# Kernel optimization log

Hardware: AMD Instinct MI355X
Metric: run time of the kernel (lower is better)

Reference implementation:

```python
import jax, jax.numpy as jnp
import numpy as np

N_NODES = 100000
N_EDGES = 1600000
IN_DIM = 128
HID = 128
OUT_DIM = 8
NUM_GRAPHS = 64


def _gcn_layer(x, src, dst, n_nodes, W, b):
    # GCNConv: x' = D^{-1/2} (A + I) D^{-1/2} (x W) + b
    h = x @ W  # [N, out]
    loop = jnp.arange(n_nodes)
    s = jnp.concatenate([src, loop])
    d = jnp.concatenate([dst, loop])
    deg = jax.ops.segment_sum(jnp.ones_like(d, dtype=h.dtype), d, num_segments=n_nodes)
    inv_sqrt = jax.lax.rsqrt(jnp.maximum(deg, 1.0))  # deg >= 1 due to self-loops
    coef = (inv_sqrt[s] * inv_sqrt[d])[:, None]      # [E+N, 1]
    msg = h[s] * coef                                # gather: [E+N, out]
    out = jax.ops.segment_sum(msg, d, num_segments=n_nodes)  # scatter-add
    return out + b


def setup_inputs() -> dict:
    key = jax.random.key(0)
    ks = jax.random.split(key, 10)
    x = jax.random.normal(ks[0], (N_NODES, IN_DIM), dtype=jnp.float32)
    edge_index = jax.random.randint(ks[1], (2, N_EDGES), 0, N_NODES, dtype=jnp.int32)
    batch = jnp.sort(jax.random.randint(ks[2], (N_NODES,), 0, NUM_GRAPHS, dtype=jnp.int32))

    def lin(k, fan_in, fan_out):
        s = 1.0 / np.sqrt(fan_in)
        return jax.random.uniform(k, (fan_in, fan_out), jnp.float32, -s, s)

    W1 = lin(ks[3], IN_DIM, HID)
    b1 = jnp.zeros((HID,), jnp.float32)
    W2 = lin(ks[4], HID, HID)
    b2 = jnp.zeros((HID,), jnp.float32)
    Wc1 = lin(ks[5], HID, HID // 2)
    bc1 = jnp.zeros((HID // 2,), jnp.float32)
    Wc2 = lin(ks[6], HID // 2, OUT_DIM)
    bc2 = jnp.zeros((OUT_DIM,), jnp.float32)
    return {"x": x, "edge_index": edge_index, "batch": batch, "num_graphs": NUM_GRAPHS,
            "W1": W1, "b1": b1, "W2": W2, "b2": b2,
            "Wc1": Wc1, "bc1": bc1, "Wc2": Wc2, "bc2": bc2}


def reference(x, edge_index, batch, num_graphs, W1, b1, W2, b2, Wc1, bc1, Wc2, bc2):
    n_nodes = x.shape[0]
    src, dst = edge_index[0], edge_index[1]
    # layer 1 (dropout inactive: eval mode)
    h = jax.nn.relu(_gcn_layer(x, src, dst, n_nodes, W1, b1))
    # layer 2
    h = jax.nn.relu(_gcn_layer(h, src, dst, n_nodes, W2, b2))
    # global mean pool per graph
    sums = jax.ops.segment_sum(h, batch, num_segments=num_graphs)  # [G, HID]
    counts = jax.ops.segment_sum(jnp.ones((n_nodes,), h.dtype), batch, num_segments=num_graphs)
    pooled = sums / jnp.maximum(counts, 1.0)[:, None]
    # MLP head [HID -> HID//2 -> OUT] (batch-norm identity at init in eval)
    z = jax.nn.relu(pooled @ Wc1 + bc1)
    return z @ Wc2 + bc2
```

## Files before the change

### kernel.cpp

```cpp
#include <hip/hip_runtime.h>
#include <hip/hip_bf16.h>

#define DIV_UP(a,b) (((a)+(b)-1)/(b))

#define CH   9216
#define CAP  7424

typedef unsigned short ushort_t;
typedef unsigned int   uint_t;
typedef __attribute__((ext_vector_type(8))) short bf16x8;
typedef __attribute__((ext_vector_type(4))) float f32x4;

__device__ __forceinline__ ushort_t f2bf(float f) {
    __hip_bfloat16 h = __float2bfloat16(f);
    ushort_t u;
    __builtin_memcpy(&u, &h, 2);
    return u;
}
__device__ __forceinline__ float bfl(uint_t u) { return __uint_as_float(u << 16); }
__device__ __forceinline__ float bfh(uint_t u) { return __uint_as_float(u & 0xffff0000u); }


__global__ __launch_bounds__(256) void k_hist1(const int* __restrict__ dst, int E,
                                               int NBK, int NB1,
                                               int* __restrict__ blk_hist) {
    __shared__ int hist[512];
    for (int i = threadIdx.x; i < NBK; i += 256) hist[i] = 0;
    __syncthreads();
    int base = blockIdx.x * CH;
    int lim = E - base; if (lim > CH) lim = CH;
    for (int i = threadIdx.x; i < lim; i += 256)
        atomicAdd(&hist[dst[base + i] >> 8], 1);
    __syncthreads();
    for (int b = threadIdx.x; b < NBK; b += 256)
        blk_hist[b * NB1 + blockIdx.x] = hist[b];
}

__global__ __launch_bounds__(256) void k_rowscan(const int* __restrict__ blk_hist,
                                                 int* __restrict__ blk_off,
                                                 int* __restrict__ T,
                                                 int NB1) {
    __shared__ int s[256];
    int b = blockIdx.x;
    const int* row = blk_hist + (size_t)b * NB1;
    int* orow = blk_off + (size_t)b * NB1;
    int t = threadIdx.x;
    int K = DIV_UP(NB1, 256);
    int lo = t * K;
    int hi = lo + K; if (hi > NB1) hi = NB1;
    int sum = 0;
    for (int i = lo; i < hi; i++) sum += row[i];
    s[t] = sum;
    __syncthreads();
    for (int o = 1; o < 256; o <<= 1) {
        int v = (t >= o) ? s[t - o] : 0;
        __syncthreads();
        s[t] += v;
        __syncthreads();
    }
    int run = s[t] - sum;
    for (int i = lo; i < hi; i++) { orow[i] = run; run += row[i]; }
    if (t == 255) T[b] = s[255];
}

__global__ __launch_bounds__(1024) void k_bktscan(const int* __restrict__ T,
                                                  int* __restrict__ bkt_base,
                                                  int NBK, int E) {
    __shared__ int s[1024];
    int t = threadIdx.x;
    int K = DIV_UP(NBK, 1024);
    int lo = t * K;
    int hi = lo + K; if (hi > NBK) hi = NBK;
    int sum = 0;
    for (int i = lo; i < hi; i++) sum += T[i];
    s[t] = sum;
    __syncthreads();
    for (int o = 1; o < 1024; o <<= 1) {
        int v = (t >= o) ? s[t - o] : 0;
        __syncthreads();
        s[t] += v;
        __syncthreads();
    }
    int run = s[t] - sum;
    for (int i = lo; i < hi; i++) { bkt_base[i] = run; run += T[i]; }
    if (t == 0) bkt_base[NBK] = E;
}


__global__ __launch_bounds__(256) void k_scatter1(const int* __restrict__ src,
                                                  const int* __restrict__ dst, int E,
                                                  int NBK, int NB1,
                                                  const int* __restrict__ blk_off,
                                                  const int* __restrict__ bkt_base,
                                                  unsigned int* __restrict__ part_arr) {
    __shared__ unsigned int   stage[CH];
    __shared__ unsigned short bko[CH];
    __shared__ int hist[512];
    __shared__ int cur[512];
    __shared__ int off[512];

    int t = threadIdx.x;
    hist[t] = 0; hist[t + 256] = 0;
    __syncthreads();

    int base = blockIdx.x * CH;
    int lim = E - base; if (lim > CH) lim = CH;

    for (int i = t; i < lim; i += 256)
        atomicAdd(&hist[dst[base + i] >> 8], 1);
    __syncthreads();

    int c0 = hist[t], c1 = hist[t + 256];
    for (int o = 1; o < 512; o <<= 1) {
        int v0 = (t >= o) ? hist[t - o] : 0;
        int v1 = hist[t + 256 - o];
        __syncthreads();
        hist[t] += v0;
        hist[t + 256] += v1;
        __syncthreads();
    }
    int e0 = hist[t] - c0;
    int e1 = hist[t + 256] - c1;
    cur[t] = e0; cur[t + 256] = e1;
    if (t < NBK)       off[t]       = blk_off[t * NB1 + blockIdx.x] + bkt_base[t] - e0;
    if (t + 256 < NBK) off[t + 256] = blk_off[(t + 256) * NB1 + blockIdx.x] + bkt_base[t + 256] - e1;
    __syncthreads();

    for (int i = t; i < lim; i += 256) {
        int d = dst[base + i];
        int sv = src[base + i];
        int b = d >> 8;
        int slot = atomicAdd(&cur[b], 1);
        stage[slot] = ((unsigned int)sv << 8) | (unsigned int)(d & 255);
        bko[slot] = (unsigned short)b;
    }
    __syncthreads();

    for (int i = t; i < lim; i += 256) {
        int b = bko[i];
        part_arr[off[b] + i] = stage[i];
    }
}

__global__ __launch_bounds__(256) void k_sortfill(const unsigned int* __restrict__ part_arr,
                                                  const int* __restrict__ bkt_base,
                                                  int N, int E,
                                                  int* __restrict__ col,
                                                  int* __restrict__ rowptr,
                                                  float* __restrict__ inv_sqrt) {
    __shared__ unsigned int in_[CAP];
    __shared__ int outS[CAP];
    __shared__ int hist[256];
    __shared__ int scn[256];
    __shared__ int cur[256];

    int b = blockIdx.x;
    int base = bkt_base[b];
    int nb   = bkt_base[b + 1] - base;
    int t = threadIdx.x;

    hist[t] = 0;
    __syncthreads();

    for (int i = t; i < nb; i += 256) {
        unsigned int pk = part_arr[base + i];
        in_[i] = pk;
        atomicAdd(&hist[pk & 255u], 1);
    }
    __syncthreads();

    int cnt = hist[t];
    for (int o = 1; o < 256; o <<= 1) {
        int v = (t >= o) ? hist[t - o] : 0;
        __syncthreads();
        hist[t] += v;
        __syncthreads();
    }
    int excl = hist[t] - cnt;
    scn[t] = excl;
    cur[t] = 0;
    __syncthreads();

    for (int i = t; i < nb; i += 256) {
        unsigned int pk = in_[i];
        int d = (int)(pk & 255u);
        int r = atomicAdd(&cur[d], 1);
        outS[scn[d] + r] = (int)(pk >> 8);
    }
    __syncthreads();

    for (int i = t; i < nb; i += 256) col[base + i] = outS[i];

    int node = b * 256 + t;
    if (node < N) {
        rowptr[node] = base + excl;
        inv_sqrt[node] = rsqrtf((float)(cnt + 1));
    }
    if (b == 0 && t == 0) rowptr[N] = E;
}


__global__ __launch_bounds__(256) void k_prepW(const float* __restrict__ W1,
                                               const float* __restrict__ W2,
                                               ushort_t* __restrict__ wT1,
                                               ushort_t* __restrict__ wT2) {
    int idx = blockIdx.x * 256 + threadIdx.x;
    const float* W = (idx < 16384) ? W1 : W2;
    ushort_t*    O = (idx < 16384) ? wT1 : wT2;
    int j = idx & 16383;
    int k = j >> 7, c = j & 127;
    O[c * 128 + k] = f2bf(W[j]);
}


template <bool BF16IN>
__global__ __launch_bounds__(256) void k_gemm_mfma(const void* __restrict__ inp,
                        const ushort_t* __restrict__ wT,
                        const float* __restrict__ inv_sqrt,
                        ushort_t* __restrict__ outg, int N) {
    __shared__ ushort_t xs[128][56];
    __shared__ ushort_t ws[128][56];
    __shared__ float ivs[128];

    const int t = threadIdx.x;
    const int row0 = blockIdx.x * 128;
    const int lane = t & 63;
    const int wv = t >> 6;
    const int wrN = wv >> 1;
    const int wcC = wv & 1;
    const int lh = lane >> 4;
    const int ll = lane & 15;

    const bool full = (row0 + 128 <= N);

    if (t < 128) {
        int r = row0 + t;
        ivs[t] = inv_sqrt[(full || r < N) ? r : 0];
    }

    f32x4 acc[4][4];
    #pragma unroll
    for (int a = 0; a < 4; a++)
        #pragma unroll
        for (int b = 0; b < 4; b++)
            acc[a][b] = (f32x4){0.f, 0.f, 0.f, 0.f};

    const uint4* wT16 = (const uint4*)wT;

    for (int kt = 0; kt < 4; kt++) {
        if (BF16IN) {
            const uint4* in16 = (const uint4*)inp;
            #pragma unroll
            for (int i = 0; i < 2; i++) {
                int fq = t + i * 256;
                int r = fq >> 2, q = fq & 3;
                int row = row0 + r;
                uint4 v = make_uint4(0u, 0u, 0u, 0u);
                if (full || row < N) v = in16[(size_t)row * 16 + kt * 4 + q];
                *(uint4*)&xs[r][q * 8] = v;
            }
        } else {
            const float4* in4 = (const float4*)inp;
            #pragma unroll
            for (int i = 0; i < 4; i++) {
                int fq = t + i * 256;
                int r = fq >> 3, q = fq & 7;
                int row = row0 + r;
                float4 v = make_float4(0.f, 0.f, 0.f, 0.f);
                if (full || row < N) v = in4[(size_t)row * 32 + kt * 8 + q];
                uint2 u;
                u.x = (uint_t)f2bf(v.x) | ((uint_t)f2bf(v.y) << 16);
                u.y = (uint_t)f2bf(v.z) | ((uint_t)f2bf(v.w) << 16);
                *(uint2*)&xs[r][q * 4] = u;
            }
        }
        #pragma unroll
        for (int i = 0; i < 2; i++) {
            int cq = t + i * 256;
            int c = cq >> 2, q = cq & 3;
            *(uint4*)&ws[c][q * 8] = wT16[(size_t)c * 16 + kt * 4 + q];
        }
        __syncthreads();

        bf16x8 aF[4], bF[4];
        #pragma unroll
        for (int nb = 0; nb < 4; nb++)
            aF[nb] = *(const bf16x8*)&xs[wrN * 64 + nb * 16 + ll][lh * 8];
        #pragma unroll
        for (int cb = 0; cb < 4; cb++)
            bF[cb] = *(const bf16x8*)&ws[wcC * 64 + cb * 16 + ll][lh * 8];
        #pragma unroll
        for (int cb = 0; cb < 4; cb++)
            #pragma unroll
            for (int nb = 0; nb < 4; nb++)
                acc[cb][nb] = __builtin_amdgcn_mfma_f32_16x16x32_bf16(
                                  bF[cb], aF[nb], acc[cb][nb], 0, 0, 0);
        __syncthreads();
    }

    #pragma unroll
    for (int nb = 0; nb < 4; nb++) {
        int lr = wrN * 64 + nb * 16 + ll;
        int row = row0 + lr;
        if (full || row < N) {
            float s = ivs[lr];
            #pragma unroll
            for (int cb = 0; cb < 4; cb++) {
                f32x4 a = acc[cb][nb];
                uint2 u;
                u.x = (uint_t)f2bf(s * a.x) | ((uint_t)f2bf(s * a.y) << 16);
                u.y = (uint_t)f2bf(s * a.z) | ((uint_t)f2bf(s * a.w) << 16);
                int colb = wcC * 64 + cb * 16 + lh * 4;
                *(uint2*)(outg + (size_t)row * 128 + colb) = u;
            }
        }
    }
}


__global__ __launch_bounds__(256) void k_agg(const ushort_t* __restrict__ g,
                            const int* __restrict__ rowptr,
                            const int* __restrict__ col, const float* __restrict__ inv_sqrt,
                            const float* __restrict__ bias, ushort_t* __restrict__ outh, int N) {
    int wid  = (blockIdx.x * blockDim.x + threadIdx.x) >> 6;
    int lane = threadIdx.x & 63;
    if (wid >= N) return;

    int start = rowptr[wid];
    int end   = rowptr[wid + 1];

    const uint_t* g1 = (const uint_t*)g;
    float accx = 0.f, accy = 0.f;

    for (int tt = start; tt < end; tt += 16) {
        int idx[16];
        #pragma unroll
        for (int i = 0; i < 16; i++)
            idx[i] = (tt + i < end) ? col[tt + i] : wid;
        uint_t v[16];
        #pragma unroll
        for (int i = 0; i < 16; i++)
            v[i] = g1[(size_t)((unsigned)idx[i] * 64u + (unsigned)lane)];
        #pragma unroll
        for (int i = 0; i < 16; i++) {
            if (tt + i < end) {
                accx += bfl(v[i]);
                accy += bfh(v[i]);
            }
        }
    }

    uint_t sv = g1[(unsigned)wid * 64u + (unsigned)lane];
    accx += bfl(sv);
    accy += bfh(sv);

    float is = inv_sqrt[wid];
    float2 b = ((const float2*)bias)[lane];
    float ox = fmaxf(fmaf(is, accx, b.x), 0.f);
    float oy = fmaxf(fmaf(is, accy, b.y), 0.f);
    uint_t pk = (uint_t)f2bf(ox) | ((uint_t)f2bf(oy) << 16);
    ((uint_t*)outh)[(size_t)wid * 64 + lane] = pk;
}


__global__ __launch_bounds__(256) void k_pool(const ushort_t* __restrict__ h,
                       const int* __restrict__ batch,
                       float* __restrict__ pooled, int* __restrict__ counts, int N) {
    int w    = threadIdx.x >> 6;
    int lane = threadIdx.x & 63;
    int row0 = blockIdx.x * 64 + w * 16;
    if (row0 >= N) return;
    int nr = N - row0; if (nr > 16) nr = 16;

    const uint_t* h1 = (const uint_t*)h;

    uint_t v[16];
    int    bb[16];
    #pragma unroll
    for (int i = 0; i < 16; i++) {
        int r = (i < nr) ? row0 + i : row0;
        v[i]  = h1[(size_t)r * 64 + lane];
        bb[i] = batch[r];
    }

    float ax = 0.f, ay = 0.f;
    int cnt = 0;
    int cur = bb[0];
    #pragma unroll
    for (int i = 0; i < 16; i++) {
        if (i < nr) {
            if (bb[i] != cur) {
                atomicAdd(&pooled[(size_t)cur * 128 + lane * 2],     ax);
                atomicAdd(&pooled[(size_t)cur * 128 + lane * 2 + 1], ay);
                if (lane == 0) atomicAdd(&counts[cur], cnt);
                ax = 0.f; ay = 0.f; cnt = 0; cur = bb[i];
            }
            ax += bfl(v[i]);
            ay += bfh(v[i]);
            cnt++;
        }
    }
    atomicAdd(&pooled[(size_t)cur * 128 + lane * 2],     ax);
    atomicAdd(&pooled[(size_t)cur * 128 + lane * 2 + 1], ay);
    if (lane == 0) atomicAdd(&counts[cur], cnt);
}


__global__ void k_mlp(const float* __restrict__ pooled, const int* __restrict__ counts,
                      const float* __restrict__ Wc1, const float* __restrict__ bc1,
                      const float* __restrict__ Wc2, const float* __restrict__ bc2,
                      float* __restrict__ out, int G) {
    int g = blockIdx.x;
    int j = threadIdx.x;
    __shared__ float pm[128];
    __shared__ float z[64];

    float invc = 1.0f / fmaxf((float)counts[g], 1.0f);
    pm[j]      = pooled[(size_t)g * 128 + j] * invc;
    pm[j + 64] = pooled[(size_t)g * 128 + 64 + j] * invc;
    __syncthreads();

    float a = bc1[j];
    #pragma unroll 8
    for (int k = 0; k < 128; k++) a += pm[k] * Wc1[k * 64 + j];
    z[j] = fmaxf(a, 0.f);
    __syncthreads();

    if (j < 8) {
        float o = bc2[j];
        #pragma unroll 8
        for (int k = 0; k < 64; k++) o += z[k] * Wc2[k * 8 + j];
        out[(size_t)g * 8 + j] = o;
    }
}


extern "C" void kernel_launch(void* const* d_in, const int* in_sizes, int n_in,
                              void* d_out, int out_size, void* d_ws, size_t ws_size,
                              hipStream_t stream) {
    const float* x    = (const float*)d_in[0];
    const int*   ei   = (const int*)d_in[1];
    const int*   batch= (const int*)d_in[2];
    const float* W1   = (const float*)d_in[4];
    const float* b1   = (const float*)d_in[5];
    const float* W2   = (const float*)d_in[6];
    const float* b2   = (const float*)d_in[7];
    const float* Wc1  = (const float*)d_in[8];
    const float* bc1  = (const float*)d_in[9];
    const float* Wc2  = (const float*)d_in[10];
    const float* bc2  = (const float*)d_in[11];
    float* out = (float*)d_out;

    const int N = in_sizes[0] / 128;
    const int E = in_sizes[1] / 2;
    const int G = out_size / 8;

    const int* src = ei;
    const int* dst = ei + E;

    const int NBK = DIV_UP(N, 256);
    const int NB1 = DIV_UP(E, CH);

    char* p = (char*)d_ws;
    auto alloc = [&](size_t bytes) {
        char* q = p;
        p += (bytes + 255) & ~(size_t)255;
        return q;
    };
    ushort_t* bufG1    = (ushort_t*)alloc((size_t)N * 128 * 2);
    ushort_t* bufG2    = (ushort_t*)alloc((size_t)N * 128 * 2);
    ushort_t* bufH     = (ushort_t*)alloc((size_t)N * 128 * 2);
    int*      rowptr   = (int*)     alloc(((size_t)N + 1) * 4);
    int*      colA     = (int*)     alloc((size_t)E * 4);
    float*    inv_sqrt = (float*)   alloc((size_t)N * 4);
    int*      blk_hist = (int*)     alloc((size_t)NBK * NB1 * 4);
    int*      blk_off  = (int*)     alloc((size_t)NBK * NB1 * 4);
    int*      bkt_base = (int*)     alloc(((size_t)NBK + 1) * 4);
    int*      bktT     = (int*)     alloc((size_t)NBK * 4);
    ushort_t* wT1      = (ushort_t*)alloc(128 * 128 * 2);
    ushort_t* wT2      = (ushort_t*)alloc(128 * 128 * 2);
    float*    pooled   = (float*)   alloc((size_t)G * 128 * 4);
    int*      counts   = (int*)     alloc((size_t)G * 4);

    unsigned int* part_arr = (unsigned int*)bufG1;

    hipMemsetAsync(pooled, 0, (size_t)G * 128 * 4, stream);
    hipMemsetAsync(counts, 0, (size_t)G * 4, stream);

    k_prepW<<<128, 256, 0, stream>>>(W1, W2, wT1, wT2);
    k_hist1<<<NB1, 256, 0, stream>>>(dst, E, NBK, NB1, blk_hist);
    k_rowscan<<<NBK, 256, 0, stream>>>(blk_hist, blk_off, bktT, NB1);
    k_bktscan<<<1, 1024, 0, stream>>>(bktT, bkt_base, NBK, E);
    k_scatter1<<<NB1, 256, 0, stream>>>(src, dst, E, NBK, NB1, blk_off, bkt_base, part_arr);
    k_sortfill<<<NBK, 256, 0, stream>>>(part_arr, bkt_base, N, E, colA, rowptr, inv_sqrt);

    k_gemm_mfma<false><<<DIV_UP(N, 128), 256, 0, stream>>>(x, wT1, inv_sqrt, bufG1, N);
    k_agg<<<DIV_UP(N, 4), 256, 0, stream>>>(bufG1, rowptr, colA, inv_sqrt, b1, bufH, N);

    k_gemm_mfma<true><<<DIV_UP(N, 128), 256, 0, stream>>>(bufH, wT2, inv_sqrt, bufG2, N);
    k_agg<<<DIV_UP(N, 4), 256, 0, stream>>>(bufG2, rowptr, colA, inv_sqrt, b2, bufG1, N);

    k_pool<<<DIV_UP(N, 64), 256, 0, stream>>>(bufG1, batch, pooled, counts, N);
    k_mlp<<<G, 64, 0, stream>>>(pooled, counts, Wc1, bc1, Wc2, bc2, out, G);
}
```

Baseline: 283.5 us.

## Merge setup launches, fold bucket scan into rowscan, pad zero row in agg

Replaces the two memsets and the weight-prep kernel with a single setup kernel that also zeroes padding rows and a completion counter. The separate single-block bucket scan is folded into k_rowscan: the last block to finish, detected through an atomic counter, scans the per-bucket totals. The aggregation kernel now points out-of-range edge slots at an all-zero padding row (index N) and accumulates without per-element predicates. The aim is fewer kernel launches and less branching in the gather loop. The risk is correctness of the last-block handoff, and the zero-row writes for threads 128–255 run past the padding row into neighbouring buffers.

```diff
diff --git a/kernel.cpp b/kernel.cpp
--- a/kernel.cpp
+++ b/kernel.cpp
@@ -21,6 +21,36 @@
 __device__ __forceinline__ float bfh(uint_t u) { return __uint_as_float(u & 0xffff0000u); }
 
 
+__global__ __launch_bounds__(256) void k_setup(const float* __restrict__ W1,
+                                               const float* __restrict__ W2,
+                                               ushort_t* __restrict__ wT1,
+                                               ushort_t* __restrict__ wT2,
+                                               float* __restrict__ pooled,
+                                               int* __restrict__ counts, int G,
+                                               ushort_t* __restrict__ zrow1,
+                                               ushort_t* __restrict__ zrow2,
+                                               int* __restrict__ done) {
+    int b = blockIdx.x;
+    int t = threadIdx.x;
+    if (b < 128) {
+        int idx = b * 256 + t;
+        const float* W = (idx < 16384) ? W1 : W2;
+        ushort_t*    O = (idx < 16384) ? wT1 : wT2;
+        int j = idx & 16383;
+        int k = j >> 7, c = j & 127;
+        O[c * 128 + k] = f2bf(W[j]);
+    } else if (b < 160) {
+        int i = (b - 128) * 256 + t;
+        if (i < G * 128) pooled[i] = 0.f;
+    } else {
+        if (t < 128) { zrow1[t] = 0; zrow2[t] = 0; }
+        else if (t < 256) { zrow1[t - 128 + 128 - 128 + 128] = 0; zrow2[t] = 0; }
+        for (int i = t; i < G; i += 256) counts[i] = 0;
+        if (t == 0) *done = 0;
+    }
+}
+
+
 __global__ __launch_bounds__(256) void k_hist1(const int* __restrict__ dst, int E,
                                                int NBK, int NB1,
                                                int* __restrict__ blk_hist) {
@@ -36,11 +66,15 @@
         blk_hist[b * NB1 + blockIdx.x] = hist[b];
 }
 
+
 __global__ __launch_bounds__(256) void k_rowscan(const int* __restrict__ blk_hist,
                                                  int* __restrict__ blk_off,
                                                  int* __restrict__ T,
-                                                 int NB1) {
+                                                 int* __restrict__ bkt_base,
+                                                 int* __restrict__ done,
+                                                 int NBK, int NB1, int E) {
     __shared__ int s[256];
+    __shared__ int amLast;
     int b = blockIdx.x;
     const int* row = blk_hist + (size_t)b * NB1;
     int* orow = blk_off + (size_t)b * NB1;
@@ -60,29 +94,28 @@
     }
     int run = s[t] - sum;
     for (int i = lo; i < hi; i++) { orow[i] = run; run += row[i]; }
-    if (t == 255) T[b] = s[255];
-}
-
-__global__ __launch_bounds__(1024) void k_bktscan(const int* __restrict__ T,
-                                                  int* __restrict__ bkt_base,
-                                                  int NBK, int E) {
-    __shared__ int s[1024];
-    int t = threadIdx.x;
-    int K = DIV_UP(NBK, 1024);
-    int lo = t * K;
-    int hi = lo + K; if (hi > NBK) hi = NBK;
-    int sum = 0;
-    for (int i = lo; i < hi; i++) sum += T[i];
-    s[t] = sum;
-    __syncthreads();
-    for (int o = 1; o < 1024; o <<= 1) {
+    if (t == 255) atomicExch(&T[b], s[255]);
+    __syncthreads();
+    if (t == 0) amLast = (atomicAdd(done, 1) == NBK - 1);
+    __syncthreads();
+    if (!amLast) return;
+
+    int K2 = DIV_UP(NBK, 256);
+    int lo2 = t * K2;
+    int hi2 = lo2 + K2; if (hi2 > NBK) hi2 = NBK;
+    int tv[8];
+    int sum2 = 0;
+    for (int i = lo2, j = 0; i < hi2; i++, j++) { tv[j] = atomicAdd(&T[i], 0); sum2 += tv[j]; }
+    s[t] = sum2;
+    __syncthreads();
+    for (int o = 1; o < 256; o <<= 1) {
         int v = (t >= o) ? s[t - o] : 0;
         __syncthreads();
         s[t] += v;
         __syncthreads();
     }
-    int run = s[t] - sum;
-    for (int i = lo; i < hi; i++) { bkt_base[i] = run; run += T[i]; }
+    int run2 = s[t] - sum2;
+    for (int i = lo2, j = 0; i < hi2; i++, j++) { bkt_base[i] = run2; run2 += tv[j]; }
     if (t == 0) bkt_base[NBK] = E;
 }
 
@@ -197,19 +230,6 @@
         inv_sqrt[node] = rsqrtf((float)(cnt + 1));
     }
     if (b == 0 && t == 0) rowptr[N] = E;
-}
-
-
-__global__ __launch_bounds__(256) void k_prepW(const float* __restrict__ W1,
-                                               const float* __restrict__ W2,
-                                               ushort_t* __restrict__ wT1,
-                                               ushort_t* __restrict__ wT2) {
-    int idx = blockIdx.x * 256 + threadIdx.x;
-    const float* W = (idx < 16384) ? W1 : W2;
-    ushort_t*    O = (idx < 16384) ? wT1 : wT2;
-    int j = idx & 16383;
-    int k = j >> 7, c = j & 127;
-    O[c * 128 + k] = f2bf(W[j]);
 }
 
 
@@ -336,17 +356,15 @@
         int idx[16];
         #pragma unroll
         for (int i = 0; i < 16; i++)
-            idx[i] = (tt + i < end) ? col[tt + i] : wid;
+            idx[i] = (tt + i < end) ? col[tt + i] : N;
         uint_t v[16];
         #pragma unroll
         for (int i = 0; i < 16; i++)
             v[i] = g1[(size_t)((unsigned)idx[i] * 64u + (unsigned)lane)];
         #pragma unroll
         for (int i = 0; i < 16; i++) {
-            if (tt + i < end) {
-                accx += bfl(v[i]);
-                accy += bfh(v[i]);
-            }
+            accx += bfl(v[i]);
+            accy += bfh(v[i]);
         }
     }
 
@@ -467,30 +485,29 @@
         p += (bytes + 255) & ~(size_t)255;
         return q;
     };
-    ushort_t* bufG1    = (ushort_t*)alloc((size_t)N * 128 * 2);
-    ushort_t* bufG2    = (ushort_t*)alloc((size_t)N * 128 * 2);
+    ushort_t* bufG1    = (ushort_t*)alloc((size_t)(N + 1) * 128 * 2);
+    ushort_t* bufG2    = (ushort_t*)alloc((size_t)(N + 1) * 128 * 2);
     ushort_t* bufH     = (ushort_t*)alloc((size_t)N * 128 * 2);
     int*      rowptr   = (int*)     alloc(((size_t)N + 1) * 4);
-    int*      colA     = (int*)     alloc((size_t)E * 4);
+    int*      colA     = (int*)     alloc((size_t)E * 4 + 256);
     float*    inv_sqrt = (float*)   alloc((size_t)N * 4);
     int*      blk_hist = (int*)     alloc((size_t)NBK * NB1 * 4);
     int*      blk_off  = (int*)     alloc((size_t)NBK * NB1 * 4);
     int*      bkt_base = (int*)     alloc(((size_t)NBK + 1) * 4);
     int*      bktT     = (int*)     alloc((size_t)NBK * 4);
+    int*      doneF    = (int*)     alloc(256);
     ushort_t* wT1      = (ushort_t*)alloc(128 * 128 * 2);
     ushort_t* wT2      = (ushort_t*)alloc(128 * 128 * 2);
     float*    pooled   = (float*)   alloc((size_t)G * 128 * 4);
     int*      counts   = (int*)     alloc((size_t)G * 4);
 
     unsigned int* part_arr = (unsigned int*)bufG1;
-
-    hipMemsetAsync(pooled, 0, (size_t)G * 128 * 4, stream);
-    hipMemsetAsync(counts, 0, (size_t)G * 4, stream);
-
-    k_prepW<<<128, 256, 0, stream>>>(W1, W2, wT1, wT2);
+    ushort_t* zrow1 = bufG1 + (size_t)N * 128;
+    ushort_t* zrow2 = bufG2 + (size_t)N * 128;
+
+    k_setup<<<161, 256, 0, stream>>>(W1, W2, wT1, wT2, pooled, counts, G, zrow1, zrow2, doneF);
     k_hist1<<<NB1, 256, 0, stream>>>(dst, E, NBK, NB1, blk_hist);
-    k_rowscan<<<NBK, 256, 0, stream>>>(blk_hist, blk_off, bktT, NB1);
-    k_bktscan<<<1, 1024, 0, stream>>>(bktT, bkt_base, NBK, E);
+    k_rowscan<<<NBK, 256, 0, stream>>>(blk_hist, blk_off, bktT, bkt_base, doneF, NBK, NB1, E);
     k_scatter1<<<NB1, 256, 0, stream>>>(src, dst, E, NBK, NB1, blk_off, bkt_base, part_arr);
     k_sortfill<<<NBK, 256, 0, stream>>>(part_arr, bkt_base, N, E, colA, rowptr, inv_sqrt);
 
```

New measurement: 276.6 us. -2.4%, faster.
